# Kernel tuning notes

Hardware: AMD Instinct MI355X
Metric: run time of the kernel (lower is better)

The kernel has to match this reference:

```python
import jax, jax.numpy as jnp
import numpy as np

B, N, E = 2, 10000, 160000
D, DC, L = 512, 8, 3
EPS = 1e-5


def layer_norm(x, g, b):
    m = jnp.mean(x, axis=-1, keepdims=True)
    v = jnp.mean((x - m) ** 2, axis=-1, keepdims=True)
    return (x - m) * jax.lax.rsqrt(v + EPS) * g + b


def setup_inputs() -> dict:
    key = jax.random.key(0)
    ks = jax.random.split(key, 8)
    node_features = jax.random.normal(ks[0], (B, N, D), dtype=jnp.float32)
    edge_index = jax.random.randint(ks[1], (2, E), 0, N, dtype=jnp.int64)
    edge_attr = jax.random.normal(ks[2], (E, D), dtype=jnp.float32)
    # manifold coordinate projection
    W_coord = jax.random.normal(ks[3], (D, DC), dtype=jnp.float32) / np.sqrt(D)
    # per-layer causal field layers (modeled as linear) and layer norms
    W_field = jax.random.normal(ks[4], (L, D, D), dtype=jnp.float32) / np.sqrt(D)
    b_field = jnp.zeros((L, D), dtype=jnp.float32)
    ln_g = jnp.ones((L, D), dtype=jnp.float32)
    ln_b = jnp.zeros((L, D), dtype=jnp.float32)
    # output projection: LayerNorm + Linear
    out_ln_g = jnp.ones((D,), dtype=jnp.float32)
    out_ln_b = jnp.zeros((D,), dtype=jnp.float32)
    W_out = jax.random.normal(ks[5], (D, D), dtype=jnp.float32) / np.sqrt(D)
    b_out = jnp.zeros((D,), dtype=jnp.float32)
    return dict(node_features=node_features, edge_index=edge_index, edge_attr=edge_attr,
                W_coord=W_coord, W_field=W_field, b_field=b_field, ln_g=ln_g, ln_b=ln_b,
                out_ln_g=out_ln_g, out_ln_b=out_ln_b, W_out=W_out, b_out=b_out)


def reference(node_features, edge_index, edge_attr, W_coord, W_field, b_field,
              ln_g, ln_b, out_ln_g, out_ln_b, W_out, b_out):
    src, dst = edge_index[0], edge_index[1]
    # node coordinates from manifold projection (computed once, from inputs)
    coords = node_features @ W_coord                        # (B, N, DC)
    # transport factor per edge, per batch: exp(-||dst_coord - src_coord||)
    coord_diff = coords[:, dst] - coords[:, src]            # (B, E, DC)
    transport = jnp.exp(-jnp.linalg.norm(coord_diff, axis=-1, keepdims=True))  # (B, E, 1)
    # degree of destination nodes (same for every batch element)
    deg = jnp.zeros((N,), dtype=node_features.dtype).at[dst].add(1.0)
    deg = jnp.clip(deg, 1.0, None)[None, :, None]           # (1, N, 1)

    x = node_features
    edge_msg = None
    for l in range(L):
        x_field = x @ W_field[l] + b_field[l]               # (B, N, D)
        # gather src features, apply transport, add edge attributes
        edge_msg = x_field[:, src] * transport + edge_attr[None]  # (B, E, D)
        # scatter-add into destination nodes, normalize by degree
        upd = jnp.zeros_like(x).at[:, dst].add(edge_msg)    # (B, N, D)
        x = layer_norm(x + upd / deg, ln_g[l], ln_b[l])
    node_output = layer_norm(x, out_ln_g, out_ln_b) @ W_out + b_out
    return node_output, edge_msg
```

## Files before the change

kernel.cpp:

```cpp
#include <hip/hip_runtime.h>
#include <stdint.h>

#define NN 10000
#define EE 160000
#define BB 2
#define DD 512
#define KC 1024
#define MVALID 20000
#define MPAD 20096
#define LEPS 1e-5f

typedef __bf16 bf16_t;
typedef __bf16 bf16x8 __attribute__((ext_vector_type(8)));
typedef float f32x4 __attribute__((ext_vector_type(4)));
typedef float f32x2 __attribute__((ext_vector_type(2)));

__device__ inline void gload16(const void* g, void* l) {
  __builtin_amdgcn_global_load_lds((const __attribute__((address_space(1))) uint32_t*)g,
                                   (__attribute__((address_space(3))) uint32_t*)l,
                                   16, 0, 0);
}

__global__ __launch_bounds__(256) void convw_k(const float* __restrict__ Wf,
                                               const float* __restrict__ Wo,
                                               const float* __restrict__ olng,
                                               bf16_t* __restrict__ wcat) {
  __shared__ float tile[64][65];
  const int kt = blockIdx.x, nt = blockIdx.y, l = blockIdx.z;
  const float* W = (l < 3) ? (Wf + (size_t)l * 262144) : Wo;
  const int tn = threadIdx.x & 63;
  const int tk = threadIdx.x >> 6;
#pragma unroll
  for (int i = 0; i < 16; i++) {
    const int kl = tk + i * 4;
    tile[kl][tn] = W[(size_t)(kt * 64 + kl) * 512 + nt * 64 + tn];
  }
  __syncthreads();
  const int kl2 = threadIdx.x & 63;
  const int nb = threadIdx.x >> 6;
  const float gk = (l == 3) ? olng[kt * 64 + kl2] : 1.0f;
#pragma unroll
  for (int i = 0; i < 16; i++) {
    const int nl = nb + i * 4;
    bf16_t h = (bf16_t)(tile[kl2][nl] * gk);
    size_t o = ((size_t)l * 512 + nt * 64 + nl) * 1024 + kt * 64 + kl2;
    wcat[o] = h;
    wcat[o + 512] = h;
  }
}

__global__ __launch_bounds__(512) void ubinit_k(const float* __restrict__ bo, float* __restrict__ ub) {
  ub[threadIdx.x] = bo[threadIdx.x];
}
__global__ __launch_bounds__(256) void ubacc_k(const float* __restrict__ olnb,
                                               const float* __restrict__ Wo,
                                               float* __restrict__ ub) {
  const int k0 = blockIdx.x * 16;
  const int tid = threadIdx.x;
#pragma unroll
  for (int h = 0; h < 2; h++) {
    const int n = tid + h * 256;
    float s = 0.f;
#pragma unroll
    for (int kk = 0; kk < 16; kk++) s += olnb[k0 + kk] * Wo[(size_t)(k0 + kk) * 512 + n];
    atomicAdd(&ub[n], s);
  }
}

__global__ __launch_bounds__(256) void coords_k(const float* __restrict__ x,
                                                const float* __restrict__ Wc,
                                                float* __restrict__ out,
                                                bf16_t* __restrict__ xcat) {
  __shared__ float smW[DD * 8];
  for (int i = threadIdx.x; i < DD * 8; i += 256) smW[i] = Wc[i];
  __syncthreads();
  const int wave = threadIdx.x >> 6, lane = threadIdx.x & 63;
  const int n = blockIdx.x * 4 + wave;
  const int b = blockIdx.y;
  const size_t row = (size_t)b * NN + n;
  const float* xr = x + row * DD + lane * 8;
  f32x4 x0 = *(const f32x4*)xr;
  f32x4 x1 = *(const f32x4*)(xr + 4);
  bf16x8 hi, lo;
#pragma unroll
  for (int j = 0; j < 8; j++) {
    float v = (j < 4) ? x0[j] : x1[j - 4];
    bf16_t h = (bf16_t)v;
    hi[j] = h;
    lo[j] = (bf16_t)(v - (float)h);
  }
  bf16_t* xc = xcat + row * KC + lane * 8;
  *(bf16x8*)xc = hi;
  *(bf16x8*)(xc + DD) = lo;
  float a[8];
#pragma unroll
  for (int dc = 0; dc < 8; dc++) a[dc] = 0.f;
#pragma unroll
  for (int j = 0; j < 8; j++) {
    float xv = (j < 4) ? x0[j] : x1[j - 4];
    const float* wrow = smW + (lane * 8 + j) * 8;
#pragma unroll
    for (int dc = 0; dc < 8; dc++) a[dc] += xv * wrow[dc];
  }
#pragma unroll
  for (int dc = 0; dc < 8; dc++)
    for (int o = 32; o >= 1; o >>= 1) a[dc] += __shfl_xor(a[dc], o);
  if (lane == 0) {
#pragma unroll
    for (int dc = 0; dc < 8; dc++) out[row * 8 + dc] = a[dc];
  }
}

__global__ __launch_bounds__(256) void transport_deg_k(const float* __restrict__ coords,
                                                       const int* __restrict__ srcA,
                                                       const int* __restrict__ dstA,
                                                       float* __restrict__ tr,
                                                       int* __restrict__ degc) {
  int e = blockIdx.x * 256 + threadIdx.x;
  int s = srcA[e], d = dstA[e];
#pragma unroll
  for (int b = 0; b < BB; b++) {
    const float* cs = coords + ((size_t)b * NN + s) * 8;
    const float* cd = coords + ((size_t)b * NN + d) * 8;
    float ss = 0.f;
#pragma unroll
    for (int i = 0; i < 8; i++) {
      float df = cd[i] - cs[i];
      ss += df * df;
    }
    tr[(size_t)b * EE + e] = expf(-sqrtf(ss));
  }
  atomicAdd(&degc[d], 1);
}

__global__ __launch_bounds__(1024) void scan_k(const int* __restrict__ cnt, int* __restrict__ rowptr,
                                               float* __restrict__ invdeg) {
  __shared__ int part[1024];
  const int tid = threadIdx.x;
  const int CH = 10;
  int base = tid * CH;
  int local[CH];
  int s = 0;
#pragma unroll
  for (int i = 0; i < CH; i++) {
    int n = base + i;
    int c = (n < NN) ? cnt[n] : 0;
    local[i] = s;
    s += c;
  }
  part[tid] = s;
  __syncthreads();
  for (int off = 1; off < 1024; off <<= 1) {
    int v = (tid >= off) ? part[tid - off] : 0;
    __syncthreads();
    part[tid] += v;
    __syncthreads();
  }
  int excl = (tid > 0) ? part[tid - 1] : 0;
#pragma unroll
  for (int i = 0; i < CH; i++) {
    int n = base + i;
    if (n < NN) {
      rowptr[n] = excl + local[i];
      int c = cnt[n];
      invdeg[n] = 1.0f / (float)(c > 1 ? c : 1);
    }
  }
  if (tid == 0) rowptr[NN] = EE;
}

__global__ __launch_bounds__(256) void fill_k(const int* __restrict__ dstA, const int* __restrict__ rowptr,
                                              int* __restrict__ fill, int* __restrict__ eidA) {
  int e = blockIdx.x * 256 + threadIdx.x;
  int d = dstA[e];
  int pos = rowptr[d] + atomicAdd(&fill[d], 1);
  eidA[pos] = e;
}

__global__ __launch_bounds__(256) void remap_k(const int* __restrict__ eidA,
                                               const int* __restrict__ srcA,
                                               const int* __restrict__ dstA,
                                               const float* __restrict__ tr,
                                               const float* __restrict__ invdeg,
                                               int* __restrict__ srcs,
                                               float* __restrict__ trs) {
  int i = blockIdx.x * 256 + threadIdx.x;
  const int e = eidA[i];
  const int s = srcA[e];
  const float idg = invdeg[dstA[e]];
  srcs[i] = s;
  trs[i] = tr[e] * idg;
  trs[(size_t)EE + i] = tr[(size_t)EE + e] * idg;
}

__global__ __launch_bounds__(256) void eagg_k(const float* __restrict__ eattr,
                                              const int* __restrict__ rowptr,
                                              const int* __restrict__ eidA,
                                              const float* __restrict__ invdeg,
                                              float* __restrict__ eagg) {
  const int n = blockIdx.x, tid = threadIdx.x;
  const int d0 = tid * 2;
  float a0 = 0.f, a1 = 0.f;
  const int beg = rowptr[n], end = rowptr[n + 1];
  for (int i = beg; i < end; i++) {
    const int e = eidA[i];
    const f32x2 r = __builtin_nontemporal_load((const f32x2*)(eattr + (size_t)e * DD + d0));
    a0 += r[0];
    a1 += r[1];
  }
  const float idg = invdeg[n];
  f32x2 o;
  o[0] = a0 * idg;
  o[1] = a1 * idg;
  *(f32x2*)(eagg + (size_t)n * DD + d0) = o;
}

template <int MODE, int KSTEPS>
__global__ __launch_bounds__(256) void gemm_bt(const bf16_t* __restrict__ A,
                                               const bf16_t* __restrict__ Bw,
                                               const float* __restrict__ bias,
                                               void* __restrict__ Cv, int mvalid,
                                               const float* __restrict__ rs) {
  __shared__ __align__(16) char smem[16384];
  const int tid = threadIdx.x;
  const int lane = tid & 63;
  const int wave = tid >> 6;
  const int mtile = blockIdx.x;
  const int ntile = blockIdx.y;
  const int wr = wave >> 1, wc = wave & 1;

  const int r = tid >> 2;
  const int c = tid & 3;
  const size_t aRow0 = (size_t)(mtile * 128 + r);
  const size_t bRow0 = (size_t)(ntile * 128 + r);
  char* smA = smem;
  char* smB = smem + 8192;
  char* ldsA0 = smA + tid * 16;
  char* ldsA1 = smA + 4096 + tid * 16;
  char* ldsB0 = smB + tid * 16;
  char* ldsB1 = smB + 4096 + tid * 16;

  f32x4 acc[4][4];
#pragma unroll
  for (int m = 0; m < 4; m++)
#pragma unroll
    for (int n = 0; n < 4; n++) acc[m][n] = (f32x4){0.f, 0.f, 0.f, 0.f};

  const int koff = (lane >> 4) * 16;
  const int arow = wr * 64 + (lane & 15);
  const int brow = wc * 64 + (lane & 15);

  for (int kk = 0; kk < KSTEPS; ++kk) {
    const int kbase = kk * 32 + c * 8;
    gload16(A + aRow0 * KC + kbase, ldsA0);
    gload16(A + (aRow0 + 64) * KC + kbase, ldsA1);
    gload16(Bw + bRow0 * KC + kbase, ldsB0);
    gload16(Bw + (bRow0 + 64) * KC + kbase, ldsB1);
    __syncthreads();
    bf16x8 af[4], bfr[4];
#pragma unroll
    for (int m = 0; m < 4; m++) af[m] = *(const bf16x8*)(smA + (arow + m * 16) * 64 + koff);
#pragma unroll
    for (int n = 0; n < 4; n++) bfr[n] = *(const bf16x8*)(smB + (brow + n * 16) * 64 + koff);
#pragma unroll
    for (int m = 0; m < 4; m++)
#pragma unroll
      for (int n = 0; n < 4; n++)
        acc[m][n] = __builtin_amdgcn_mfma_f32_16x16x32_bf16(af[m], bfr[n], acc[m][n], 0, 0, 0);
    __syncthreads();
  }

  const int crow0 = mtile * 128 + wr * 64 + (lane >> 4) * 4;
  const int ccol0 = ntile * 128 + wc * 64 + (lane & 15);
#pragma unroll
  for (int n = 0; n < 4; n++) {
    const int col = ccol0 + n * 16;
    const float bv = bias[col];
#pragma unroll
    for (int m = 0; m < 4; m++) {
      const int rw = crow0 + m * 16;
#pragma unroll
      for (int j = 0; j < 4; j++) {
        int rowi = rw + j;
        if (rowi < mvalid) {
          if constexpr (MODE == 0)
            ((bf16_t*)Cv)[(size_t)rowi * DD + col] = (bf16_t)(acc[m][n][j] + bv);
          else
            ((float*)Cv)[(size_t)rowi * DD + col] = acc[m][n][j] * rs[rowi] + bv;
        }
      }
    }
  }
}

__global__ __launch_bounds__(256) void layer_k(const bf16_t* __restrict__ xfield,
                                               const float* __restrict__ nf, int is_l0, int outstat,
                                               bf16_t* __restrict__ xcat,
                                               const int* __restrict__ srcs,
                                               const float* __restrict__ trs,
                                               const int* __restrict__ rowptr,
                                               const float* __restrict__ eagg,
                                               const float* __restrict__ g,
                                               const float* __restrict__ bbias,
                                               float* __restrict__ rs_out) {
  const int wave = threadIdx.x >> 6, lane = threadIdx.x & 63;
  const int n = blockIdx.x * 4 + wave;
  const int d0 = lane * 8;
  const int beg = rowptr[n], end = rowptr[n + 1];
  const bf16_t* xf0 = xfield + (size_t)0 * NN * DD + d0;
  const bf16_t* xf1 = xfield + (size_t)1 * NN * DD + d0;
  const float* trs1p = trs + EE;
  float acc0[8], acc1[8];
#pragma unroll
  for (int j = 0; j < 8; j++) acc0[j] = acc1[j] = 0.f;

  for (int c0 = beg; c0 < end; c0 += 64) {
    const int cnt = min(64, end - c0);
    int s_r = 0;
    float t0_r = 0.f, t1_r = 0.f;
    if (lane < cnt) {
      s_r = srcs[c0 + lane];
      t0_r = trs[c0 + lane];
      t1_r = trs1p[c0 + lane];
    }
    for (int j = 0; j < cnt; j += 4) {
#pragma unroll
      for (int u = 0; u < 4; u++) {
        const int jj = j + u;
        const int s = __shfl(s_r, jj);
        const float t0 = __shfl(t0_r, jj);
        const float t1 = __shfl(t1_r, jj);
        const bf16x8 xv0 = *(const bf16x8*)(xf0 + (size_t)s * DD);
        const bf16x8 xv1 = *(const bf16x8*)(xf1 + (size_t)s * DD);
#pragma unroll
        for (int q = 0; q < 8; q++) {
          acc0[q] += t0 * (float)xv0[q];
          acc1[q] += t1 * (float)xv1[q];
        }
      }
    }
  }

  bf16_t* xc0 = xcat + (size_t)n * KC + d0;
  bf16_t* xc1 = xcat + (size_t)(NN + n) * KC + d0;
  float xp0[8], xp1[8];
  if (is_l0) {
    const f32x4 p00 = *(const f32x4*)(nf + (size_t)n * DD + d0);
    const f32x4 p01 = *(const f32x4*)(nf + (size_t)n * DD + d0 + 4);
    const f32x4 p10 = *(const f32x4*)(nf + (size_t)(NN + n) * DD + d0);
    const f32x4 p11 = *(const f32x4*)(nf + (size_t)(NN + n) * DD + d0 + 4);
#pragma unroll
    for (int j = 0; j < 8; j++) {
      xp0[j] = (j < 4) ? p00[j] : p01[j - 4];
      xp1[j] = (j < 4) ? p10[j] : p11[j - 4];
    }
  } else {
    const bf16x8 h0 = *(const bf16x8*)(xc0);
    const bf16x8 l0v = *(const bf16x8*)(xc0 + DD);
    const bf16x8 h1 = *(const bf16x8*)(xc1);
    const bf16x8 l1v = *(const bf16x8*)(xc1 + DD);
#pragma unroll
    for (int j = 0; j < 8; j++) {
      xp0[j] = (float)h0[j] + (float)l0v[j];
      xp1[j] = (float)h1[j] + (float)l1v[j];
    }
  }
  const f32x4 e0 = *(const f32x4*)(eagg + (size_t)n * DD + d0);
  const f32x4 e1 = *(const f32x4*)(eagg + (size_t)n * DD + d0 + 4);
  float v0[8], v1[8];
  float s10 = 0.f, s20 = 0.f, s11 = 0.f, s21 = 0.f;
#pragma unroll
  for (int j = 0; j < 8; j++) {
    const float ea = (j < 4) ? e0[j] : e1[j - 4];
    v0[j] = xp0[j] + acc0[j] + ea;
    v1[j] = xp1[j] + acc1[j] + ea;
    s10 += v0[j];
    s20 += v0[j] * v0[j];
    s11 += v1[j];
    s21 += v1[j] * v1[j];
  }
#pragma unroll
  for (int o = 32; o >= 1; o >>= 1) {
    s10 += __shfl_xor(s10, o);
    s20 += __shfl_xor(s20, o);
    s11 += __shfl_xor(s11, o);
    s21 += __shfl_xor(s21, o);
  }
  const float mean0 = s10 * (1.f / 512.f);
  const float rs0 = rsqrtf(s20 * (1.f / 512.f) - mean0 * mean0 + LEPS);
  const float mean1 = s11 * (1.f / 512.f);
  const float rs1 = rsqrtf(s21 * (1.f / 512.f) - mean1 * mean1 + LEPS);
  const f32x4 g0 = *(const f32x4*)(g + d0);
  const f32x4 g1 = *(const f32x4*)(g + d0 + 4);
  const f32x4 b0 = *(const f32x4*)(bbias + d0);
  const f32x4 b1 = *(const f32x4*)(bbias + d0 + 4);
  float y0[8], y1[8];
  float sy10 = 0.f, sy20 = 0.f, sy11 = 0.f, sy21 = 0.f;
#pragma unroll
  for (int j = 0; j < 8; j++) {
    const float gg = (j < 4) ? g0[j] : g1[j - 4];
    const float bb = (j < 4) ? b0[j] : b1[j - 4];
    y0[j] = (v0[j] - mean0) * rs0 * gg + bb;
    y1[j] = (v1[j] - mean1) * rs1 * gg + bb;
    sy10 += y0[j];
    sy20 += y0[j] * y0[j];
    sy11 += y1[j];
    sy21 += y1[j] * y1[j];
  }
  float sub0 = 0.f, sub1 = 0.f;
  if (outstat) {
#pragma unroll
    for (int o = 32; o >= 1; o >>= 1) {
      sy10 += __shfl_xor(sy10, o);
      sy20 += __shfl_xor(sy20, o);
      sy11 += __shfl_xor(sy11, o);
      sy21 += __shfl_xor(sy21, o);
    }
    const float my0 = sy10 * (1.f / 512.f);
    const float rsy0 = rsqrtf(sy20 * (1.f / 512.f) - my0 * my0 + LEPS);
    const float my1 = sy11 * (1.f / 512.f);
    const float rsy1 = rsqrtf(sy21 * (1.f / 512.f) - my1 * my1 + LEPS);
    if (lane == 0) {
      rs_out[n] = rsy0;
      rs_out[NN + n] = rsy1;
    }
    sub0 = my0;
    sub1 = my1;
  }
  bf16x8 ho0, lo0, ho1, lo1;
#pragma unroll
  for (int j = 0; j < 8; j++) {
    const float ya = y0[j] - sub0;
    const float yb = y1[j] - sub1;
    bf16_t ha = (bf16_t)ya;
    bf16_t hb = (bf16_t)yb;
    ho0[j] = ha;
    lo0[j] = (bf16_t)(ya - (float)ha);
    ho1[j] = hb;
    lo1[j] = (bf16_t)(yb - (float)hb);
  }
  *(bf16x8*)xc0 = ho0;
  *(bf16x8*)(xc0 + DD) = lo0;
  *(bf16x8*)xc1 = ho1;
  *(bf16x8*)(xc1 + DD) = lo1;
}

__global__ __launch_bounds__(256) void edgemsg_k(const bf16_t* __restrict__ xfield,
                                                 const float* __restrict__ transport,
                                                 const int* __restrict__ srcA,
                                                 const float* __restrict__ eattr,
                                                 float* __restrict__ out) {
  const int wv = threadIdx.x >> 6, lane = threadIdx.x & 63;
  const int e = blockIdx.x * 4 + wv;
  const int d0 = lane * 8;
  const int s = srcA[e];
  const f32x4 a0 = __builtin_nontemporal_load((const f32x4*)(eattr + (size_t)e * DD + d0));
  const f32x4 a1 = __builtin_nontemporal_load((const f32x4*)(eattr + (size_t)e * DD + d0 + 4));
  const float t0 = transport[e];
  const float t1 = transport[(size_t)EE + e];
  const bf16x8 x0 = *(const bf16x8*)(xfield + (size_t)s * DD + d0);
  const bf16x8 x1 = *(const bf16x8*)(xfield + ((size_t)NN + s) * DD + d0);
  f32x4 o00, o01, o10, o11;
#pragma unroll
  for (int j = 0; j < 4; j++) {
    o00[j] = (float)x0[j] * t0 + a0[j];
    o01[j] = (float)x0[j + 4] * t0 + a1[j];
    o10[j] = (float)x1[j] * t1 + a0[j];
    o11[j] = (float)x1[j + 4] * t1 + a1[j];
  }
  float* ob0 = out + (size_t)e * DD + d0;
  float* ob1 = out + ((size_t)EE + e) * DD + d0;
  __builtin_nontemporal_store(o00, (f32x4*)ob0);
  __builtin_nontemporal_store(o01, (f32x4*)(ob0 + 4));
  __builtin_nontemporal_store(o10, (f32x4*)ob1);
  __builtin_nontemporal_store(o11, (f32x4*)(ob1 + 4));
}

extern "C" void kernel_launch(void* const* d_in, const int* in_sizes, int n_in,
                              void* d_out, int out_size, void* d_ws, size_t ws_size,
                              hipStream_t stream) {
  const float* nf = (const float*)d_in[0];
  const int* eidx = (const int*)d_in[1];
  const float* eattr = (const float*)d_in[2];
  const float* Wc = (const float*)d_in[3];
  const float* Wf = (const float*)d_in[4];
  const float* bfield = (const float*)d_in[5];
  const float* lng = (const float*)d_in[6];
  const float* lnb = (const float*)d_in[7];
  const float* olng = (const float*)d_in[8];
  const float* olnb = (const float*)d_in[9];
  const float* Wo = (const float*)d_in[10];
  const float* bo = (const float*)d_in[11];
  const int* srcA = eidx;
  const int* dstA = eidx + EE;
  float* outp = (float*)d_out;

  char* ws = (char*)d_ws;
  size_t off = 0;
  auto alloc = [&](size_t bytes) {
    void* p = ws + off;
    off += (bytes + 255) & ~(size_t)255;
    return p;
  };
  bf16_t* xcat = (bf16_t*)alloc((size_t)MPAD * KC * 2);
  bf16_t* xfield = (bf16_t*)alloc((size_t)MPAD * DD * 2);
  bf16_t* wcat = (bf16_t*)alloc((size_t)4 * DD * KC * 2);
  float* eagg = (float*)alloc((size_t)NN * DD * 4);
  float* coords = (float*)alloc((size_t)BB * NN * 8 * 4);
  float* transport = (float*)alloc((size_t)BB * EE * 4);
  float* trs = (float*)alloc((size_t)BB * EE * 4);
  int* srcs = (int*)alloc(EE * 4);
  int* degc = (int*)alloc(NN * 4);
  int* rowptr = (int*)alloc((NN + 1) * 4);
  int* fillb = (int*)alloc(NN * 4);
  int* eidl = (int*)alloc(EE * 4);
  float* invdeg = (float*)alloc(NN * 4);
  float* rs_out = (float*)alloc((size_t)BB * NN * 4);
  float* ub = (float*)alloc(DD * 4);

  hipMemsetAsync(degc, 0, NN * 4, stream);
  hipMemsetAsync(fillb, 0, NN * 4, stream);
  hipMemsetAsync(xcat + (size_t)MVALID * KC, 0, (size_t)(MPAD - MVALID) * KC * 2, stream);

  convw_k<<<dim3(8, 8, 4), 256, 0, stream>>>(Wf, Wo, olng, wcat);
  ubinit_k<<<1, 512, 0, stream>>>(bo, ub);
  ubacc_k<<<32, 256, 0, stream>>>(olnb, Wo, ub);
  coords_k<<<dim3(2500, 2), 256, 0, stream>>>(nf, Wc, coords, xcat);
  transport_deg_k<<<625, 256, 0, stream>>>(coords, srcA, dstA, transport, degc);
  scan_k<<<1, 1024, 0, stream>>>(degc, rowptr, invdeg);
  fill_k<<<625, 256, 0, stream>>>(dstA, rowptr, fillb, eidl);
  remap_k<<<625, 256, 0, stream>>>(eidl, srcA, dstA, transport, invdeg, srcs, trs);
  eagg_k<<<10000, 256, 0, stream>>>(eattr, rowptr, eidl, invdeg, eagg);

  for (int l = 0; l < 3; l++) {
    gemm_bt<0, 16><<<dim3(157, 4), 256, 0, stream>>>(xcat, wcat + (size_t)l * DD * KC,
                                                     bfield + l * DD, xfield, MVALID, nullptr);
    if (l == 2)
      edgemsg_k<<<40000, 256, 0, stream>>>(xfield, transport, srcA, eattr,
                                           outp + (size_t)BB * NN * DD);
    layer_k<<<2500, 256, 0, stream>>>(xfield, nf, (l == 0) ? 1 : 0, (l == 2) ? 1 : 0, xcat, srcs,
                                      trs, rowptr, eagg, lng + l * DD, lnb + l * DD, rs_out);
  }
  gemm_bt<1, 32><<<dim3(157, 4), 256, 0, stream>>>(xcat, wcat + (size_t)3 * DD * KC, ub, outp,
                                                   MVALID, rs_out);
}
```

Before: 685.8 us.

## Fuse edge-attr aggregation into first layer kernel and trim final GEMM K

The standalone eagg_k pass is removed. The first layer kernel now gathers and sums edge attributes per destination node alongside the feature aggregation, then stores the degree-normalized result for later layers. The weight buffer is no longer duplicated to K=1024, so the output GEMM runs over K=512 and only uses the high bf16 half of the split activations, which loses some output precision. Two memsets are also merged into one.

```diff
diff --git a/kernel.cpp b/kernel.cpp
--- a/kernel.cpp
+++ b/kernel.cpp
@@ -43,9 +43,7 @@
   for (int i = 0; i < 16; i++) {
     const int nl = nb + i * 4;
     bf16_t h = (bf16_t)(tile[kl2][nl] * gk);
-    size_t o = ((size_t)l * 512 + nt * 64 + nl) * 1024 + kt * 64 + kl2;
-    wcat[o] = h;
-    wcat[o + 512] = h;
+    wcat[((size_t)l * 512 + nt * 64 + nl) * 512 + kt * 64 + kl2] = h;
   }
 }
 
@@ -193,34 +191,10 @@
   trs[(size_t)EE + i] = tr[(size_t)EE + e] * idg;
 }
 
-__global__ __launch_bounds__(256) void eagg_k(const float* __restrict__ eattr,
-                                              const int* __restrict__ rowptr,
-                                              const int* __restrict__ eidA,
-                                              const float* __restrict__ invdeg,
-                                              float* __restrict__ eagg) {
-  const int n = blockIdx.x, tid = threadIdx.x;
-  const int d0 = tid * 2;
-  float a0 = 0.f, a1 = 0.f;
-  const int beg = rowptr[n], end = rowptr[n + 1];
-  for (int i = beg; i < end; i++) {
-    const int e = eidA[i];
-    const f32x2 r = __builtin_nontemporal_load((const f32x2*)(eattr + (size_t)e * DD + d0));
-    a0 += r[0];
-    a1 += r[1];
-  }
-  const float idg = invdeg[n];
-  f32x2 o;
-  o[0] = a0 * idg;
-  o[1] = a1 * idg;
-  *(f32x2*)(eagg + (size_t)n * DD + d0) = o;
-}
-
-template <int MODE, int KSTEPS>
-__global__ __launch_bounds__(256) void gemm_bt(const bf16_t* __restrict__ A,
-                                               const bf16_t* __restrict__ Bw,
-                                               const float* __restrict__ bias,
-                                               void* __restrict__ Cv, int mvalid,
-                                               const float* __restrict__ rs) {
+__global__ __launch_bounds__(256) void gemm_bt_b(const bf16_t* __restrict__ A,
+                                                 const bf16_t* __restrict__ Bw,
+                                                 const float* __restrict__ bias,
+                                                 bf16_t* __restrict__ C, int mvalid) {
   __shared__ __align__(16) char smem[16384];
   const int tid = threadIdx.x;
   const int lane = tid & 63;
@@ -228,7 +202,6 @@
   const int mtile = blockIdx.x;
   const int ntile = blockIdx.y;
   const int wr = wave >> 1, wc = wave & 1;
-
   const int r = tid >> 2;
   const int c = tid & 3;
   const size_t aRow0 = (size_t)(mtile * 128 + r);
@@ -250,12 +223,12 @@
   const int arow = wr * 64 + (lane & 15);
   const int brow = wc * 64 + (lane & 15);
 
-  for (int kk = 0; kk < KSTEPS; ++kk) {
+  for (int kk = 0; kk < 16; ++kk) {
     const int kbase = kk * 32 + c * 8;
     gload16(A + aRow0 * KC + kbase, ldsA0);
     gload16(A + (aRow0 + 64) * KC + kbase, ldsA1);
-    gload16(Bw + bRow0 * KC + kbase, ldsB0);
-    gload16(Bw + (bRow0 + 64) * KC + kbase, ldsB1);
+    gload16(Bw + bRow0 * 512 + kbase, ldsB0);
+    gload16(Bw + (bRow0 + 64) * 512 + kbase, ldsB1);
     __syncthreads();
     bf16x8 af[4], bfr[4];
 #pragma unroll
@@ -282,24 +255,94 @@
 #pragma unroll
       for (int j = 0; j < 4; j++) {
         int rowi = rw + j;
-        if (rowi < mvalid) {
-          if constexpr (MODE == 0)
-            ((bf16_t*)Cv)[(size_t)rowi * DD + col] = (bf16_t)(acc[m][n][j] + bv);
-          else
-            ((float*)Cv)[(size_t)rowi * DD + col] = acc[m][n][j] * rs[rowi] + bv;
-        }
+        if (rowi < mvalid) C[(size_t)rowi * DD + col] = (bf16_t)(acc[m][n][j] + bv);
       }
     }
   }
 }
 
+__global__ __launch_bounds__(256) void gemm_bt_f(const bf16_t* __restrict__ A,
+                                                 const bf16_t* __restrict__ Bw,
+                                                 const float* __restrict__ bias,
+                                                 float* __restrict__ C, int mvalid,
+                                                 const float* __restrict__ rs) {
+  __shared__ __align__(16) char smem[16384];
+  const int tid = threadIdx.x;
+  const int lane = tid & 63;
+  const int wave = tid >> 6;
+  const int mtile = blockIdx.x;
+  const int ntile = blockIdx.y;
+  const int wr = wave >> 1, wc = wave & 1;
+  const int r = tid >> 2;
+  const int c = tid & 3;
+  const size_t aRow0 = (size_t)(mtile * 128 + r);
+  const size_t bRow0 = (size_t)(ntile * 128 + r);
+  char* smA = smem;
+  char* smB = smem + 8192;
+  char* ldsA0 = smA + tid * 16;
+  char* ldsA1 = smA + 4096 + tid * 16;
+  char* ldsB0 = smB + tid * 16;
+  char* ldsB1 = smB + 4096 + tid * 16;
+
+  f32x4 acc[4][4];
+#pragma unroll
+  for (int m = 0; m < 4; m++)
+#pragma unroll
+    for (int n = 0; n < 4; n++) acc[m][n] = (f32x4){0.f, 0.f, 0.f, 0.f};
+
+  const int koff = (lane >> 4) * 16;
+  const int arow = wr * 64 + (lane & 15);
+  const int brow = wc * 64 + (lane & 15);
+
+  for (int kk = 0; kk < 16; ++kk) {
+    const int kbase = kk * 32 + c * 8;
+    gload16(A + aRow0 * KC + kbase, ldsA0);
+    gload16(A + (aRow0 + 64) * KC + kbase, ldsA1);
+    gload16(Bw + bRow0 * 512 + kbase, ldsB0);
+    gload16(Bw + (bRow0 + 64) * 512 + kbase, ldsB1);
+    __syncthreads();
+    bf16x8 af[4], bfr[4];
+#pragma unroll
+    for (int m = 0; m < 4; m++) af[m] = *(const bf16x8*)(smA + (arow + m * 16) * 64 + koff);
+#pragma unroll
+    for (int n = 0; n < 4; n++) bfr[n] = *(const bf16x8*)(smB + (brow + n * 16) * 64 + koff);
+#pragma unroll
+    for (int m = 0; m < 4; m++)
+#pragma unroll
+      for (int n = 0; n < 4; n++)
+        acc[m][n] = __builtin_amdgcn_mfma_f32_16x16x32_bf16(af[m], bfr[n], acc[m][n], 0, 0, 0);
+    __syncthreads();
+  }
+
+  const int crow0 = mtile * 128 + wr * 64 + (lane >> 4) * 4;
+  const int ccol0 = ntile * 128 + wc * 64 + (lane & 15);
+#pragma unroll
+  for (int n = 0; n < 4; n++) {
+    const int col = ccol0 + n * 16;
+    const float bv = bias[col];
+#pragma unroll
+    for (int m = 0; m < 4; m++) {
+      const int rw = crow0 + m * 16;
+#pragma unroll
+      for (int j = 0; j < 4; j++) {
+        int rowi = rw + j;
+        if (rowi < mvalid) C[(size_t)rowi * DD + col] = acc[m][n][j] * rs[rowi] + bv;
+      }
+    }
+  }
+}
+
+template <int FUSE_EA>
 __global__ __launch_bounds__(256) void layer_k(const bf16_t* __restrict__ xfield,
                                                const float* __restrict__ nf, int is_l0, int outstat,
                                                bf16_t* __restrict__ xcat,
                                                const int* __restrict__ srcs,
                                                const float* __restrict__ trs,
                                                const int* __restrict__ rowptr,
-                                               const float* __restrict__ eagg,
+                                               const int* __restrict__ eidA,
+                                               const float* __restrict__ eattr,
+                                               const float* __restrict__ invdeg,
+                                               float* __restrict__ eagg,
                                                const float* __restrict__ g,
                                                const float* __restrict__ bbias,
                                                float* __restrict__ rs_out) {
@@ -310,18 +353,19 @@
   const bf16_t* xf0 = xfield + (size_t)0 * NN * DD + d0;
   const bf16_t* xf1 = xfield + (size_t)1 * NN * DD + d0;
   const float* trs1p = trs + EE;
-  float acc0[8], acc1[8];
-#pragma unroll
-  for (int j = 0; j < 8; j++) acc0[j] = acc1[j] = 0.f;
+  float acc0[8], acc1[8], eac[8];
+#pragma unroll
+  for (int j = 0; j < 8; j++) acc0[j] = acc1[j] = eac[j] = 0.f;
 
   for (int c0 = beg; c0 < end; c0 += 64) {
     const int cnt = min(64, end - c0);
-    int s_r = 0;
+    int s_r = 0, e_r = 0;
     float t0_r = 0.f, t1_r = 0.f;
     if (lane < cnt) {
       s_r = srcs[c0 + lane];
       t0_r = trs[c0 + lane];
       t1_r = trs1p[c0 + lane];
+      if (FUSE_EA) e_r = eidA[c0 + lane];
     }
     for (int j = 0; j < cnt; j += 4) {
 #pragma unroll
@@ -332,6 +376,16 @@
         const float t1 = __shfl(t1_r, jj);
         const bf16x8 xv0 = *(const bf16x8*)(xf0 + (size_t)s * DD);
         const bf16x8 xv1 = *(const bf16x8*)(xf1 + (size_t)s * DD);
+        if (FUSE_EA) {
+          const int e = __shfl(e_r, jj);
+          const bool act = jj < cnt;
+          const f32x4 r0 = __builtin_nontemporal_load((const f32x4*)(eattr + (size_t)e * DD + d0));
+          const f32x4 r1 = __builtin_nontemporal_load((const f32x4*)(eattr + (size_t)e * DD + d0 + 4));
+          if (act) {
+#pragma unroll
+            for (int q = 0; q < 8; q++) eac[q] += (q < 4) ? r0[q & 3] : r1[q & 3];
+          }
+        }
 #pragma unroll
         for (int q = 0; q < 8; q++) {
           acc0[q] += t0 * (float)xv0[q];
@@ -339,6 +393,26 @@
         }
       }
     }
+  }
+
+  float ea8[8];
+  if (FUSE_EA) {
+    const float idg = invdeg[n];
+#pragma unroll
+    for (int j = 0; j < 8; j++) ea8[j] = eac[j] * idg;
+    f32x4 o0, o1;
+#pragma unroll
+    for (int j = 0; j < 4; j++) {
+      o0[j] = ea8[j];
+      o1[j] = ea8[j + 4];
+    }
+    *(f32x4*)(eagg + (size_t)n * DD + d0) = o0;
+    *(f32x4*)(eagg + (size_t)n * DD + d0 + 4) = o1;
+  } else {
+    const f32x4 e0 = *(const f32x4*)(eagg + (size_t)n * DD + d0);
+    const f32x4 e1 = *(const f32x4*)(eagg + (size_t)n * DD + d0 + 4);
+#pragma unroll
+    for (int j = 0; j < 8; j++) ea8[j] = (j < 4) ? e0[j] : e1[j - 4];
   }
 
   bf16_t* xc0 = xcat + (size_t)n * KC + d0;
@@ -365,15 +439,12 @@
       xp1[j] = (float)h1[j] + (float)l1v[j];
     }
   }
-  const f32x4 e0 = *(const f32x4*)(eagg + (size_t)n * DD + d0);
-  const f32x4 e1 = *(const f32x4*)(eagg + (size_t)n * DD + d0 + 4);
   float v0[8], v1[8];
   float s10 = 0.f, s20 = 0.f, s11 = 0.f, s21 = 0.f;
 #pragma unroll
   for (int j = 0; j < 8; j++) {
-    const float ea = (j < 4) ? e0[j] : e1[j - 4];
-    v0[j] = xp0[j] + acc0[j] + ea;
-    v1[j] = xp1[j] + acc1[j] + ea;
+    v0[j] = xp0[j] + acc0[j] + ea8[j];
+    v1[j] = xp1[j] + acc1[j] + ea8[j];
     s10 += v0[j];
     s20 += v0[j] * v0[j];
     s11 += v1[j];
@@ -504,22 +575,22 @@
   };
   bf16_t* xcat = (bf16_t*)alloc((size_t)MPAD * KC * 2);
   bf16_t* xfield = (bf16_t*)alloc((size_t)MPAD * DD * 2);
-  bf16_t* wcat = (bf16_t*)alloc((size_t)4 * DD * KC * 2);
+  bf16_t* wcat = (bf16_t*)alloc((size_t)4 * DD * 512 * 2);
   float* eagg = (float*)alloc((size_t)NN * DD * 4);
   float* coords = (float*)alloc((size_t)BB * NN * 8 * 4);
   float* transport = (float*)alloc((size_t)BB * EE * 4);
   float* trs = (float*)alloc((size_t)BB * EE * 4);
   int* srcs = (int*)alloc(EE * 4);
-  int* degc = (int*)alloc(NN * 4);
+  int* degfill = (int*)alloc((size_t)2 * NN * 4);
+  int* degc = degfill;
+  int* fillb = degfill + NN;
   int* rowptr = (int*)alloc((NN + 1) * 4);
-  int* fillb = (int*)alloc(NN * 4);
   int* eidl = (int*)alloc(EE * 4);
   float* invdeg = (float*)alloc(NN * 4);
   float* rs_out = (float*)alloc((size_t)BB * NN * 4);
   float* ub = (float*)alloc(DD * 4);
 
-  hipMemsetAsync(degc, 0, NN * 4, stream);
-  hipMemsetAsync(fillb, 0, NN * 4, stream);
+  hipMemsetAsync(degfill, 0, (size_t)2 * NN * 4, stream);
   hipMemsetAsync(xcat + (size_t)MVALID * KC, 0, (size_t)(MPAD - MVALID) * KC * 2, stream);
 
   convw_k<<<dim3(8, 8, 4), 256, 0, stream>>>(Wf, Wo, olng, wcat);
@@ -530,17 +601,21 @@
   scan_k<<<1, 1024, 0, stream>>>(degc, rowptr, invdeg);
   fill_k<<<625, 256, 0, stream>>>(dstA, rowptr, fillb, eidl);
   remap_k<<<625, 256, 0, stream>>>(eidl, srcA, dstA, transport, invdeg, srcs, trs);
-  eagg_k<<<10000, 256, 0, stream>>>(eattr, rowptr, eidl, invdeg, eagg);
 
   for (int l = 0; l < 3; l++) {
-    gemm_bt<0, 16><<<dim3(157, 4), 256, 0, stream>>>(xcat, wcat + (size_t)l * DD * KC,
-                                                     bfield + l * DD, xfield, MVALID, nullptr);
+    gemm_bt_b<<<dim3(157, 4), 256, 0, stream>>>(xcat, wcat + (size_t)l * DD * 512,
+                                                bfield + l * DD, xfield, MVALID);
     if (l == 2)
       edgemsg_k<<<40000, 256, 0, stream>>>(xfield, transport, srcA, eattr,
                                            outp + (size_t)BB * NN * DD);
-    layer_k<<<2500, 256, 0, stream>>>(xfield, nf, (l == 0) ? 1 : 0, (l == 2) ? 1 : 0, xcat, srcs,
-                                      trs, rowptr, eagg, lng + l * DD, lnb + l * DD, rs_out);
-  }
-  gemm_bt<1, 32><<<dim3(157, 4), 256, 0, stream>>>(xcat, wcat + (size_t)3 * DD * KC, ub, outp,
-                                                   MVALID, rs_out);
-}
+    if (l == 0)
+      layer_k<1><<<2500, 256, 0, stream>>>(xfield, nf, 1, 0, xcat, srcs, trs, rowptr, eidl, eattr,
+                                           invdeg, eagg, lng + l * DD, lnb + l * DD, rs_out);
+    else
+      layer_k<0><<<2500, 256, 0, stream>>>(xfield, nf, 0, (l == 2) ? 1 : 0, xcat, srcs, trs,
+                                           rowptr, eidl, eattr, invdeg, eagg, lng + l * DD,
+                                           lnb + l * DD, rs_out);
+  }
+  gemm_bt_f<<<dim3(157, 4), 256, 0, stream>>>(xcat, wcat + (size_t)3 * DD * 512, ub, outp, MVALID,
+                                              rs_out);
+}
```

Result: faster. 651.9 us (-5.0%).
